# Optimization experiments

Hardware: AMD Instinct MI355X
Metric: run time of the kernel (lower is better)

The kernel has to match this reference:

```python
import jax, jax.numpy as jnp
import numpy as np


def setup_inputs() -> dict:
    key = jax.random.key(0)
    kq, kk, kv, km = jax.random.split(key, 4)
    b, h, w, c = 4, 128, 512, 128
    num_splits = 8
    win = w // num_splits  # 64
    q = jax.random.normal(kq, (b, h * w, c), dtype=jnp.float32)
    k = jax.random.normal(kk, (b, h * w, c), dtype=jnp.float32)
    v = jax.random.normal(kv, (b, h * w, c), dtype=jnp.float32)
    attn_mask = jax.random.normal(km, (num_splits, win, win), dtype=jnp.float32)
    return {"q": q, "k": k, "v": v, "attn_mask": attn_mask,
            "h": h, "w": w, "num_splits": num_splits}


def reference(q, k, v, attn_mask, h, w, num_splits):
    # with_shift=True branch (attn_mask is only consumed when shifting)
    b, hw, c = q.shape
    assert hw == h * w
    win = w // num_splits
    shift = win // 2
    scale = c ** 0.5

    def prep(x):
        # [b, h*w, c] -> rows of width w, shifted, then split into windows
        x = x.reshape(b * h, w, c)
        x = jnp.roll(x, -shift, axis=1)
        return x.reshape(b * h, num_splits, win, c)

    qs, ks, vs = prep(q), prep(k), prep(v)
    scores = jnp.einsum('bsqc,bskc->bsqk', qs, ks) / scale
    scores = scores + attn_mask[None]  # broadcast over b*h (== torch repeat)
    attn = jax.nn.softmax(scores, axis=-1)
    out = jnp.einsum('bsqk,bskc->bsqc', attn, vs)
    # merge windows back to rows: [b, h, w, c]
    out = out.reshape(b, h, w, c)
    out = jnp.roll(out, shift, axis=2)  # undo shift along w
    return out.reshape(b, h * w, c)
```

## Files before the change

### kernel.cpp

```cpp
#include <hip/hip_runtime.h>
#include <hip/hip_bf16.h>

#define BH      512
#define W_ROWS  512
#define C_DIM   128
#define NSPLIT  8
#define WIN     64
#define SHIFT   32

typedef __attribute__((ext_vector_type(8))) short  short8;
typedef __attribute__((ext_vector_type(4))) float  floatx4;

__device__ __forceinline__ ushort f2bf(float x) {
    union { float f; unsigned u; } c; c.f = x;
    unsigned u = c.u;
    return (ushort)((u + 0x7FFFu + ((u >> 16) & 1u)) >> 16);
}

__global__ __launch_bounds__(256)
void swin_attn_kernel(const float* __restrict__ qg,
                      const float* __restrict__ kg,
                      const float* __restrict__ vg,
                      const float* __restrict__ mg,
                      float* __restrict__ og)
{
    __shared__ __align__(16) ushort sK [64][136];
    __shared__ __align__(16) ushort sVt[128][72];
    __shared__ __align__(16) ushort sP [64][72];

    const int tid  = threadIdx.x;
    const int bh   = blockIdx.x >> 3;
    const int s    = blockIdx.x & 7;
    const int wv   = tid >> 6;
    const int lane = tid & 63;
    const int l16  = lane & 15;
    const int quad = lane >> 4;

    const size_t base = (size_t)bh * (W_ROWS * C_DIM);

    for (int i = 0; i < 8; ++i) {
        int idx = i * 256 + tid;
        int row = idx >> 5;
        int c0  = (idx & 31) << 2;
        int rg  = (s * WIN + row + SHIFT) & (W_ROWS - 1);
        size_t goff = base + (size_t)rg * C_DIM + c0;
        float4 kv = *(const float4*)(kg + goff);
        ushort4 kb;
        kb.x = f2bf(kv.x); kb.y = f2bf(kv.y); kb.z = f2bf(kv.z); kb.w = f2bf(kv.w);
        *(ushort4*)&sK[row][c0] = kb;
        float4 vv = *(const float4*)(vg + goff);
        sVt[c0 + 0][row] = f2bf(vv.x);
        sVt[c0 + 1][row] = f2bf(vv.y);
        sVt[c0 + 2][row] = f2bf(vv.z);
        sVt[c0 + 3][row] = f2bf(vv.w);
    }
    __syncthreads();

    floatx4 acc[4];
    const floatx4 fz = {0.f, 0.f, 0.f, 0.f};
    for (int t = 0; t < 4; ++t) acc[t] = fz;

    const int qrow = wv * 16 + l16;
    const int rgq  = (s * WIN + qrow + SHIFT) & (W_ROWS - 1);
    const float* qp = qg + base + (size_t)rgq * C_DIM + quad * 8;

    for (int kk = 0; kk < 4; ++kk) {
        float4 a0 = *(const float4*)(qp + kk * 32);
        float4 a1 = *(const float4*)(qp + kk * 32 + 4);
        short8 af;
        af[0] = (short)f2bf(a0.x); af[1] = (short)f2bf(a0.y);
        af[2] = (short)f2bf(a0.z); af[3] = (short)f2bf(a0.w);
        af[4] = (short)f2bf(a1.x); af[5] = (short)f2bf(a1.y);
        af[6] = (short)f2bf(a1.z); af[7] = (short)f2bf(a1.w);
        const int ch0 = kk * 32 + quad * 8;
        for (int t = 0; t < 4; ++t) {
            short8 bf = *(const short8*)&sK[t * 16 + l16][ch0];
            acc[t] = __builtin_amdgcn_mfma_f32_16x16x32_bf16(af, bf, acc[t], 0, 0, 0);
        }
    }

    const float* mrow = mg + s * (WIN * WIN);
    float pr[4][4];
    for (int r = 0; r < 4; ++r) {
        const int qw = wv * 16 + quad * 4 + r;
        float mx = -3.0e38f;
        for (int t = 0; t < 4; ++t) {
            float val = acc[t][r] * 0.08838834764831845f
                      + mrow[qw * WIN + t * 16 + l16];
            pr[t][r] = val;
            mx = fmaxf(mx, val);
        }
        mx = fmaxf(mx, __shfl_xor(mx, 1));
        mx = fmaxf(mx, __shfl_xor(mx, 2));
        mx = fmaxf(mx, __shfl_xor(mx, 4));
        mx = fmaxf(mx, __shfl_xor(mx, 8));
        float sum = 0.f;
        for (int t = 0; t < 4; ++t) {
            float e = __expf(pr[t][r] - mx);
            pr[t][r] = e;
            sum += e;
        }
        sum += __shfl_xor(sum, 1);
        sum += __shfl_xor(sum, 2);
        sum += __shfl_xor(sum, 4);
        sum += __shfl_xor(sum, 8);
        float rs = 1.0f / sum;
        for (int t = 0; t < 4; ++t)
            sP[qw][t * 16 + l16] = f2bf(pr[t][r] * rs);
    }
    __syncthreads();

    floatx4 o[8];
    for (int t = 0; t < 8; ++t) o[t] = fz;
    for (int kk = 0; kk < 2; ++kk) {
        short8 pf = *(const short8*)&sP[wv * 16 + l16][kk * 32 + quad * 8];
        for (int t = 0; t < 8; ++t) {
            short8 vf = *(const short8*)&sVt[t * 16 + l16][kk * 32 + quad * 8];
            o[t] = __builtin_amdgcn_mfma_f32_16x16x32_bf16(pf, vf, o[t], 0, 0, 0);
        }
    }

    for (int r = 0; r < 4; ++r) {
        const int qw = wv * 16 + quad * 4 + r;
        const int rg = (s * WIN + qw + SHIFT) & (W_ROWS - 1);
        float* op = og + base + (size_t)rg * C_DIM + l16;
        for (int t = 0; t < 8; ++t)
            op[t * 16] = o[t][r];
    }
}

extern "C" void kernel_launch(void* const* d_in, const int* in_sizes, int n_in,
                              void* d_out, int out_size, void* d_ws, size_t ws_size,
                              hipStream_t stream) {
    const float* q = (const float*)d_in[0];
    const float* k = (const float*)d_in[1];
    const float* v = (const float*)d_in[2];
    const float* m = (const float*)d_in[3];
    float* out = (float*)d_out;
    dim3 grid(BH * NSPLIT), block(256);
    hipLaunchKernelGGL(swin_attn_kernel, grid, block, 0, stream, q, k, v, m, out);
}
```

Before: 400.5 us.

## Batch global loads, swizzle transposed V stores, and alias P onto K smem

All K, V and Q global loads are now issued up front into registers so more memory requests are in flight before any bf16 conversion. The V transpose goes through registers: each thread packs 8 rows of one channel into a 16-byte vector store into an XOR-swizzled shared buffer, replacing scalar 2-byte scattered stores. The P buffer reuses the K shared memory after an extra barrier, shrinking LDS per block, and launch bounds request 4 blocks per SM. This costs more registers per thread and one additional synchronization.

Result: no change. 395.7 us (-1.2%).

```diff
diff --git a/kernel.cpp b/kernel.cpp
--- a/kernel.cpp
+++ b/kernel.cpp
@@ -1,5 +1,4 @@
 #include <hip/hip_runtime.h>
-#include <hip/hip_bf16.h>
 
 #define BH      512
 #define W_ROWS  512
@@ -17,16 +16,15 @@
     return (ushort)((u + 0x7FFFu + ((u >> 16) & 1u)) >> 16);
 }
 
-__global__ __launch_bounds__(256)
+__global__ __launch_bounds__(256, 4)
 void swin_attn_kernel(const float* __restrict__ qg,
                       const float* __restrict__ kg,
                       const float* __restrict__ vg,
                       const float* __restrict__ mg,
                       float* __restrict__ og)
 {
-    __shared__ __align__(16) ushort sK [64][136];
-    __shared__ __align__(16) ushort sVt[128][72];
-    __shared__ __align__(16) ushort sP [64][72];
+    __shared__ __align__(16) ushort sK[64][136];
+    __shared__ __align__(16) char   sVt[128 * 144];
 
     const int tid  = threadIdx.x;
     const int bh   = blockIdx.x >> 3;
@@ -38,52 +36,81 @@
 
     const size_t base = (size_t)bh * (W_ROWS * C_DIM);
 
+    const int j  = tid & 31;
+    const int h  = tid >> 5;
+    const int c0 = j * 4;
+    const int r0 = h * 8;
+
+    floatx4 kr[8], vr[8];
+    #pragma unroll
     for (int i = 0; i < 8; ++i) {
-        int idx = i * 256 + tid;
-        int row = idx >> 5;
-        int c0  = (idx & 31) << 2;
-        int rg  = (s * WIN + row + SHIFT) & (W_ROWS - 1);
-        size_t goff = base + (size_t)rg * C_DIM + c0;
-        float4 kv = *(const float4*)(kg + goff);
+        const int rg = (s * WIN + r0 + i + SHIFT) & (W_ROWS - 1);
+        kr[i] = *(const floatx4*)(kg + base + (size_t)rg * C_DIM + c0);
+    }
+    #pragma unroll
+    for (int i = 0; i < 8; ++i) {
+        const int rg = (s * WIN + r0 + i + SHIFT) & (W_ROWS - 1);
+        vr[i] = *(const floatx4*)(vg + base + (size_t)rg * C_DIM + c0);
+    }
+    const int qrow = wv * 16 + l16;
+    const int rgq  = (s * WIN + qrow + SHIFT) & (W_ROWS - 1);
+    const float* qp = qg + base + (size_t)rgq * C_DIM + quad * 8;
+    floatx4 qa[4], qb[4];
+    #pragma unroll
+    for (int kk = 0; kk < 4; ++kk) {
+        qa[kk] = *(const floatx4*)(qp + kk * 32);
+        qb[kk] = *(const floatx4*)(qp + kk * 32 + 4);
+    }
+
+    #pragma unroll
+    for (int i = 0; i < 8; ++i) {
         ushort4 kb;
-        kb.x = f2bf(kv.x); kb.y = f2bf(kv.y); kb.z = f2bf(kv.z); kb.w = f2bf(kv.w);
-        *(ushort4*)&sK[row][c0] = kb;
-        float4 vv = *(const float4*)(vg + goff);
-        sVt[c0 + 0][row] = f2bf(vv.x);
-        sVt[c0 + 1][row] = f2bf(vv.y);
-        sVt[c0 + 2][row] = f2bf(vv.z);
-        sVt[c0 + 3][row] = f2bf(vv.w);
+        kb.x = f2bf(kr[i][0]); kb.y = f2bf(kr[i][1]);
+        kb.z = f2bf(kr[i][2]); kb.w = f2bf(kr[i][3]);
+        *(ushort4*)&sK[r0 + i][c0] = kb;
+    }
+    #pragma unroll
+    for (int m = 0; m < 4; ++m) {
+        short8 col;
+        #pragma unroll
+        for (int i = 0; i < 8; ++i) col[i] = (short)f2bf(vr[i][m]);
+        const int chnk = h ^ (j & 7);
+        *(short8*)(sVt + (size_t)(c0 + m) * 144 + chnk * 16) = col;
+    }
+    short8 qf[4];
+    #pragma unroll
+    for (int kk = 0; kk < 4; ++kk) {
+        short8 f;
+        f[0] = (short)f2bf(qa[kk][0]); f[1] = (short)f2bf(qa[kk][1]);
+        f[2] = (short)f2bf(qa[kk][2]); f[3] = (short)f2bf(qa[kk][3]);
+        f[4] = (short)f2bf(qb[kk][0]); f[5] = (short)f2bf(qb[kk][1]);
+        f[6] = (short)f2bf(qb[kk][2]); f[7] = (short)f2bf(qb[kk][3]);
+        qf[kk] = f;
     }
     __syncthreads();
 
     floatx4 acc[4];
     const floatx4 fz = {0.f, 0.f, 0.f, 0.f};
+    #pragma unroll
     for (int t = 0; t < 4; ++t) acc[t] = fz;
 
-    const int qrow = wv * 16 + l16;
-    const int rgq  = (s * WIN + qrow + SHIFT) & (W_ROWS - 1);
-    const float* qp = qg + base + (size_t)rgq * C_DIM + quad * 8;
-
+    #pragma unroll
     for (int kk = 0; kk < 4; ++kk) {
-        float4 a0 = *(const float4*)(qp + kk * 32);
-        float4 a1 = *(const float4*)(qp + kk * 32 + 4);
-        short8 af;
-        af[0] = (short)f2bf(a0.x); af[1] = (short)f2bf(a0.y);
-        af[2] = (short)f2bf(a0.z); af[3] = (short)f2bf(a0.w);
-        af[4] = (short)f2bf(a1.x); af[5] = (short)f2bf(a1.y);
-        af[6] = (short)f2bf(a1.z); af[7] = (short)f2bf(a1.w);
         const int ch0 = kk * 32 + quad * 8;
+        #pragma unroll
         for (int t = 0; t < 4; ++t) {
             short8 bf = *(const short8*)&sK[t * 16 + l16][ch0];
-            acc[t] = __builtin_amdgcn_mfma_f32_16x16x32_bf16(af, bf, acc[t], 0, 0, 0);
+            acc[t] = __builtin_amdgcn_mfma_f32_16x16x32_bf16(qf[kk], bf, acc[t], 0, 0, 0);
         }
     }
 
     const float* mrow = mg + s * (WIN * WIN);
     float pr[4][4];
+    #pragma unroll
     for (int r = 0; r < 4; ++r) {
         const int qw = wv * 16 + quad * 4 + r;
         float mx = -3.0e38f;
+        #pragma unroll
         for (int t = 0; t < 4; ++t) {
             float val = acc[t][r] * 0.08838834764831845f
                       + mrow[qw * WIN + t * 16 + l16];
@@ -95,6 +122,7 @@
         mx = fmaxf(mx, __shfl_xor(mx, 4));
         mx = fmaxf(mx, __shfl_xor(mx, 8));
         float sum = 0.f;
+        #pragma unroll
         for (int t = 0; t < 4; ++t) {
             float e = __expf(pr[t][r] - mx);
             pr[t][r] = e;
@@ -105,25 +133,42 @@
         sum += __shfl_xor(sum, 4);
         sum += __shfl_xor(sum, 8);
         float rs = 1.0f / sum;
+        #pragma unroll
+        for (int t = 0; t < 4; ++t) pr[t][r] *= rs;
+    }
+
+    __syncthreads();
+    ushort* sP = (ushort*)&sK[0][0];
+    #pragma unroll
+    for (int r = 0; r < 4; ++r) {
+        const int qw = wv * 16 + quad * 4 + r;
+        #pragma unroll
         for (int t = 0; t < 4; ++t)
-            sP[qw][t * 16 + l16] = f2bf(pr[t][r] * rs);
+            sP[qw * 72 + t * 16 + l16] = f2bf(pr[t][r]);
     }
     __syncthreads();
 
     floatx4 o[8];
+    #pragma unroll
     for (int t = 0; t < 8; ++t) o[t] = fz;
+    #pragma unroll
     for (int kk = 0; kk < 2; ++kk) {
-        short8 pf = *(const short8*)&sP[wv * 16 + l16][kk * 32 + quad * 8];
+        short8 pf = *(const short8*)&sP[(wv * 16 + l16) * 72 + kk * 32 + quad * 8];
+        #pragma unroll
         for (int t = 0; t < 8; ++t) {
-            short8 vf = *(const short8*)&sVt[t * 16 + l16][kk * 32 + quad * 8];
+            const int ch   = t * 16 + l16;
+            const int chnk = (kk * 4 + quad) ^ ((ch >> 2) & 7);
+            short8 vf = *(const short8*)(sVt + (size_t)ch * 144 + chnk * 16);
             o[t] = __builtin_amdgcn_mfma_f32_16x16x32_bf16(pf, vf, o[t], 0, 0, 0);
         }
     }
 
+    #pragma unroll
     for (int r = 0; r < 4; ++r) {
         const int qw = wv * 16 + quad * 4 + r;
         const int rg = (s * WIN + qw + SHIFT) & (W_ROWS - 1);
         float* op = og + base + (size_t)rg * C_DIM + l16;
+        #pragma unroll
         for (int t = 0; t < 8; ++t)
             op[t * 16] = o[t][r];
     }
```
